# Performance work log

Hardware: AMD Instinct MI355X
Metric: run time of the kernel (lower is better)

Reference implementation:

```python
import jax, jax.numpy as jnp
import numpy as np

B = 8192
EMBED = 4  # self-attention embed dim


def setup_inputs() -> dict:
    key = jax.random.key(0)
    ks = jax.random.split(key, 20)
    f32 = jnp.float32
    return {
        "inputs": jax.random.normal(ks[0], (B, 8), dtype=f32),
        # MLP chain params (stored as [in, out]; y = x @ W + b)
        "W_fm": jax.random.normal(ks[1], (8, 16), dtype=f32) * 0.1,
        "b_fm": jnp.zeros((16,), dtype=f32),
        "W_c1": jax.random.normal(ks[2], (16, 16), dtype=f32) * 0.1,
        "b_c1": jnp.zeros((16,), dtype=f32),
        "W_p1": jax.random.normal(ks[3], (16, 12), dtype=f32) * 0.1,
        "b_p1": jnp.zeros((12,), dtype=f32),
        "W_c2": jax.random.normal(ks[4], (12, 8), dtype=f32) * 0.1,
        "b_c2": jnp.zeros((8,), dtype=f32),
        "W_p2": jax.random.normal(ks[5], (8, 4), dtype=f32) * 0.1,
        "b_p2": jnp.zeros((4,), dtype=f32),
        "W_c3": jax.random.normal(ks[6], (4, 4), dtype=f32) * 0.1,
        "b_c3": jnp.zeros((4,), dtype=f32),
        # self-attention params
        "rot": jax.random.normal(ks[7], (EMBED, EMBED), dtype=f32),
        "ent": jax.random.normal(ks[8], (EMBED, EMBED), dtype=f32),
        # ConvFilter: 2x2 conv kernel flattened (cross-correlation over 2x2 patch)
        "conv_w": jax.random.normal(ks[9], (4,), dtype=f32) * 0.5,
        "conv_b": jnp.zeros((1,), dtype=f32),
        # head: Linear(1,1)
        "head_w": jax.random.normal(ks[10], (1, 1), dtype=f32),
        "head_b": jnp.zeros((1,), dtype=f32),
    }


def reference(inputs, W_fm, b_fm, W_c1, b_c1, W_p1, b_p1, W_c2, b_c2,
              W_p2, b_p2, W_c3, b_c3, rot, ent, conv_w, conv_b,
              head_w, head_b):
    threshold = 0.0
    shift = 0.0
    # MLP chain: Linear + Tanh blocks
    x = jnp.tanh(inputs @ W_fm + b_fm)   # [B,16]
    x = jnp.tanh(x @ W_c1 + b_c1)        # [B,16]
    x = jnp.tanh(x @ W_p1 + b_p1)        # [B,12]
    x = jnp.tanh(x @ W_c2 + b_c2)        # [B,8]
    x = jnp.tanh(x @ W_p2 + b_p2)        # [B,4]
    x = jnp.tanh(x @ W_c3 + b_c3)        # [B,4]
    # self-attention over the batch axis (as in the original torch.mm)
    q = x @ rot                           # [B,4]
    k = x @ ent                           # [B,4]
    scores = jax.nn.softmax((q @ k.T) / jnp.sqrt(jnp.float32(EMBED)), axis=-1)  # [B,B]
    x = scores @ x                        # [B,4]
    # batched 2x2 conv filter: each sample's 4-vector reshaped to 2x2, one
    # valid conv output -> sum(w * patch) + b; mean of single elem is itself
    filtered = jax.nn.sigmoid(x @ conv_w + conv_b - threshold)[:, None]  # [B,1]
    logits = filtered @ head_w + head_b   # [B,1]
    return jax.nn.sigmoid(logits + shift)
```

## Files before the change

### kernel.cpp

```cpp
#include <hip/hip_runtime.h>
#include <math.h>

#define BATCH 8192
#define BLK 256
#define NSPLIT 32
#define CHUNK (BATCH / NSPLIT)


template <int IN, int OUT>
__device__ __forceinline__ void layer_tanh(const float* a, float* out,
                                           const float* __restrict__ W,
                                           const float* __restrict__ bias) {
  float acc[OUT];
#pragma unroll
  for (int o = 0; o < OUT; o++) acc[o] = bias[o];
#pragma unroll
  for (int i = 0; i < IN; i++) {
    float ai = a[i];
#pragma unroll
    for (int o = 0; o < OUT; o++) acc[o] = fmaf(ai, W[i * OUT + o], acc[o]);
  }
#pragma unroll
  for (int o = 0; o < OUT; o++) out[o] = tanhf(acc[o]);
}

__global__ __launch_bounds__(BLK) void mlp_kernel(
    const float* __restrict__ in,
    const float* __restrict__ W_fm, const float* __restrict__ b_fm,
    const float* __restrict__ W_c1, const float* __restrict__ b_c1,
    const float* __restrict__ W_p1, const float* __restrict__ b_p1,
    const float* __restrict__ W_c2, const float* __restrict__ b_c2,
    const float* __restrict__ W_p2, const float* __restrict__ b_p2,
    const float* __restrict__ W_c3, const float* __restrict__ b_c3,
    const float* __restrict__ rot, const float* __restrict__ ent,
    float4* __restrict__ qv, float4* __restrict__ kvx) {
  __shared__ float w[812];
  const int t = threadIdx.x;
  auto cp = [&](const float* src, int off, int n) {
    for (int i = t; i < n; i += BLK) w[off + i] = src[i];
  };
  cp(W_fm, 0, 128);  cp(b_fm, 128, 16);
  cp(W_c1, 144, 256); cp(b_c1, 400, 16);
  cp(W_p1, 416, 192); cp(b_p1, 608, 12);
  cp(W_c2, 620, 96);  cp(b_c2, 716, 8);
  cp(W_p2, 724, 32);  cp(b_p2, 756, 4);
  cp(W_c3, 760, 16);  cp(b_c3, 776, 4);
  cp(rot, 780, 16);   cp(ent, 796, 16);
  __syncthreads();

  const int r = blockIdx.x * BLK + t;
  const float4* in4 = (const float4*)in;
  float4 i0 = in4[r * 2 + 0];
  float4 i1 = in4[r * 2 + 1];
  float a[16], b[16];
  a[0] = i0.x; a[1] = i0.y; a[2] = i0.z; a[3] = i0.w;
  a[4] = i1.x; a[5] = i1.y; a[6] = i1.z; a[7] = i1.w;

  layer_tanh<8, 16>(a, b, w + 0, w + 128);
  layer_tanh<16, 16>(b, a, w + 144, w + 400);
  layer_tanh<16, 12>(a, b, w + 416, w + 608);
  layer_tanh<12, 8>(b, a, w + 620, w + 716);
  layer_tanh<8, 4>(a, b, w + 724, w + 756);
  layer_tanh<4, 4>(b, a, w + 760, w + 776);
  float q[4], k[4];
#pragma unroll
  for (int d = 0; d < 4; d++) {
    q[d] = a[0] * w[780 + 0 * 4 + d] + a[1] * w[780 + 1 * 4 + d] +
           a[2] * w[780 + 2 * 4 + d] + a[3] * w[780 + 3 * 4 + d];
    k[d] = a[0] * w[796 + 0 * 4 + d] + a[1] * w[796 + 1 * 4 + d] +
           a[2] * w[796 + 2 * 4 + d] + a[3] * w[796 + 3 * 4 + d];
  }
  qv[r] = make_float4(q[0] * 0.5f, q[1] * 0.5f, q[2] * 0.5f, q[3] * 0.5f);
  kvx[2 * r + 0] = make_float4(k[0], k[1], k[2], k[3]);
  kvx[2 * r + 1] = make_float4(a[0], a[1], a[2], a[3]);
}

__device__ __forceinline__ float dot4(float4 a, float4 b) {
  return fmaf(a.x, b.x, fmaf(a.y, b.y, fmaf(a.z, b.z, a.w * b.w)));
}

__global__ __launch_bounds__(BLK) void attn_partial(
    const float4* __restrict__ kvx, const float4* __restrict__ qv,
    float* __restrict__ l_arr, float4* __restrict__ o_arr) {
  const int t = threadIdx.x;
  const int qi = blockIdx.x * BLK + t;
  const int c0 = blockIdx.y * CHUNK;
  const float4 q = qv[qi];

  float l0 = 0.f, l1 = 0.f;
  float4 o0 = make_float4(0.f, 0.f, 0.f, 0.f);
  float4 o1 = make_float4(0.f, 0.f, 0.f, 0.f);
#pragma unroll 4
  for (int j = 0; j < CHUNK; j += 2) {
    const float4 ka = kvx[(c0 + j) * 2 + 0];
    const float4 va = kvx[(c0 + j) * 2 + 1];
    const float4 kb = kvx[(c0 + j) * 2 + 2];
    const float4 vb = kvx[(c0 + j) * 2 + 3];
    float s0 = dot4(q, ka);
    float s1 = dot4(q, kb);
    float p0 = __expf(s0);
    float p1 = __expf(s1);
    l0 += p0;
    l1 += p1;
    o0.x = fmaf(p0, va.x, o0.x); o0.y = fmaf(p0, va.y, o0.y);
    o0.z = fmaf(p0, va.z, o0.z); o0.w = fmaf(p0, va.w, o0.w);
    o1.x = fmaf(p1, vb.x, o1.x); o1.y = fmaf(p1, vb.y, o1.y);
    o1.z = fmaf(p1, vb.z, o1.z); o1.w = fmaf(p1, vb.w, o1.w);
  }
  const int idx = blockIdx.y * BATCH + qi;
  l_arr[idx] = l0 + l1;
  o_arr[idx] = make_float4(o0.x + o1.x, o0.y + o1.y, o0.z + o1.z, o0.w + o1.w);
}

__global__ __launch_bounds__(BLK) void combine_kernel(
    const float* __restrict__ l_arr, const float4* __restrict__ o_arr,
    const float* __restrict__ conv_w, const float* __restrict__ conv_b,
    const float* __restrict__ head_w, const float* __restrict__ head_b,
    float* __restrict__ out) {
  const int qi = blockIdx.x * BLK + threadIdx.x;
  float l = 0.f;
  float4 o = make_float4(0.f, 0.f, 0.f, 0.f);
#pragma unroll
  for (int s = 0; s < NSPLIT; s++) {
    l += l_arr[s * BATCH + qi];
    float4 os = o_arr[s * BATCH + qi];
    o.x += os.x; o.y += os.y; o.z += os.z; o.w += os.w;
  }
  const float inv = 1.0f / l;
  float z = o.x * inv * conv_w[0] + o.y * inv * conv_w[1] +
            o.z * inv * conv_w[2] + o.w * inv * conv_w[3] + conv_b[0];
  float filtered = 1.0f / (1.0f + __expf(-z));
  float logit = fmaf(filtered, head_w[0], head_b[0]);
  out[qi] = 1.0f / (1.0f + __expf(-logit));
}

extern "C" void kernel_launch(void* const* d_in, const int* in_sizes, int n_in,
                              void* d_out, int out_size, void* d_ws,
                              size_t ws_size, hipStream_t stream) {
  const float* in   = (const float*)d_in[0];
  const float* W_fm = (const float*)d_in[1];
  const float* b_fm = (const float*)d_in[2];
  const float* W_c1 = (const float*)d_in[3];
  const float* b_c1 = (const float*)d_in[4];
  const float* W_p1 = (const float*)d_in[5];
  const float* b_p1 = (const float*)d_in[6];
  const float* W_c2 = (const float*)d_in[7];
  const float* b_c2 = (const float*)d_in[8];
  const float* W_p2 = (const float*)d_in[9];
  const float* b_p2 = (const float*)d_in[10];
  const float* W_c3 = (const float*)d_in[11];
  const float* b_c3 = (const float*)d_in[12];
  const float* rot  = (const float*)d_in[13];
  const float* ent  = (const float*)d_in[14];
  const float* conv_w = (const float*)d_in[15];
  const float* conv_b = (const float*)d_in[16];
  const float* head_w = (const float*)d_in[17];
  const float* head_b = (const float*)d_in[18];
  float* out = (float*)d_out;

  char* ws = (char*)d_ws;
  float4* qv  = (float4*)(ws + 0);
  float4* kvx = (float4*)(ws + (128 << 10));
  float*  l_arr = (float*)(ws + (384 << 10));
  float4* o_arr = (float4*)(ws + (384 << 10) + NSPLIT * BATCH * 4);

  mlp_kernel<<<BATCH / BLK, BLK, 0, stream>>>(
      in, W_fm, b_fm, W_c1, b_c1, W_p1, b_p1, W_c2, b_c2, W_p2, b_p2, W_c3,
      b_c3, rot, ent, qv, kvx);

  dim3 grid(BATCH / BLK, NSPLIT);
  attn_partial<<<grid, BLK, 0, stream>>>(kvx, qv, l_arr, o_arr);

  combine_kernel<<<BATCH / BLK, BLK, 0, stream>>>(
      l_arr, o_arr, conv_w, conv_b, head_w, head_b, out);
}
```

Before: 128.3 us.

## Fuse MLP into attention kernel, recomputing query and key rows per block

Removes the separate MLP kernel. Each attention block now recomputes the MLP for its 256 query rows and its 256-key chunk, stages K/V in shared memory, and runs the partial softmax-weighted sum from LDS instead of global memory. tanhf is replaced by an exp/reciprocal approximation. Weights are read directly from global/scalar memory instead of shared memory, and launch bounds request 3 blocks per SM. The trade is redundant MLP compute (each row is recomputed 32 times as a query and 32 times as a key) in exchange for one fewer launch, no intermediate global traffic, and LDS-resident keys.

```diff
diff --git a/kernel.cpp b/kernel.cpp
--- a/kernel.cpp
+++ b/kernel.cpp
@@ -6,25 +6,44 @@
 #define NSPLIT 32
 #define CHUNK (BATCH / NSPLIT)
 
+__device__ __forceinline__ float tanh_fast(float x) {
+  float e = __expf(x + x);
+  return fmaf(-2.0f, __builtin_amdgcn_rcpf(e + 1.0f), 1.0f);
+}
 
 template <int IN, int OUT>
-__device__ __forceinline__ void layer_tanh(const float* a, float* out,
-                                           const float* __restrict__ W,
-                                           const float* __restrict__ bias) {
-  float acc[OUT];
+__device__ __forceinline__ void layer2_tanh(
+    const float* x0, const float* x1, float* y0, float* y1,
+    const float* __restrict__ W, const float* __restrict__ bias) {
+  float acc0[OUT], acc1[OUT];
 #pragma unroll
-  for (int o = 0; o < OUT; o++) acc[o] = bias[o];
+  for (int o = 0; o < OUT; o++) {
+    float b = bias[o];
+    acc0[o] = b;
+    acc1[o] = b;
+  }
 #pragma unroll
   for (int i = 0; i < IN; i++) {
-    float ai = a[i];
+    float a0 = x0[i], a1 = x1[i];
 #pragma unroll
-    for (int o = 0; o < OUT; o++) acc[o] = fmaf(ai, W[i * OUT + o], acc[o]);
+    for (int o = 0; o < OUT; o++) {
+      float w = W[i * OUT + o];
+      acc0[o] = fmaf(a0, w, acc0[o]);
+      acc1[o] = fmaf(a1, w, acc1[o]);
+    }
   }
 #pragma unroll
-  for (int o = 0; o < OUT; o++) out[o] = tanhf(acc[o]);
+  for (int o = 0; o < OUT; o++) {
+    y0[o] = tanh_fast(acc0[o]);
+    y1[o] = tanh_fast(acc1[o]);
+  }
 }
 
-__global__ __launch_bounds__(BLK) void mlp_kernel(
+__device__ __forceinline__ float dot4(float4 a, float4 b) {
+  return fmaf(a.x, b.x, fmaf(a.y, b.y, fmaf(a.z, b.z, a.w * b.w)));
+}
+
+__global__ __launch_bounds__(BLK, 3) void fused_attn(
     const float* __restrict__ in,
     const float* __restrict__ W_fm, const float* __restrict__ b_fm,
     const float* __restrict__ W_c1, const float* __restrict__ b_c1,
@@ -33,71 +52,57 @@
     const float* __restrict__ W_p2, const float* __restrict__ b_p2,
     const float* __restrict__ W_c3, const float* __restrict__ b_c3,
     const float* __restrict__ rot, const float* __restrict__ ent,
-    float4* __restrict__ qv, float4* __restrict__ kvx) {
-  __shared__ float w[812];
+    float* __restrict__ l_arr, float4* __restrict__ o_arr) {
+  __shared__ float4 kv[2 * CHUNK];
+
   const int t = threadIdx.x;
-  auto cp = [&](const float* src, int off, int n) {
-    for (int i = t; i < n; i += BLK) w[off + i] = src[i];
-  };
-  cp(W_fm, 0, 128);  cp(b_fm, 128, 16);
-  cp(W_c1, 144, 256); cp(b_c1, 400, 16);
-  cp(W_p1, 416, 192); cp(b_p1, 608, 12);
-  cp(W_c2, 620, 96);  cp(b_c2, 716, 8);
-  cp(W_p2, 724, 32);  cp(b_p2, 756, 4);
-  cp(W_c3, 760, 16);  cp(b_c3, 776, 4);
-  cp(rot, 780, 16);   cp(ent, 796, 16);
+  const int qi = blockIdx.x * BLK + t;
+  const int ki = blockIdx.y * CHUNK + t;
+
+  const float4* in4 = (const float4*)in;
+  float4 A0 = in4[2 * qi + 0], A1 = in4[2 * qi + 1];
+  float4 B0 = in4[2 * ki + 0], B1 = in4[2 * ki + 1];
+
+  float xq[16], tq[16], xk[16], tk[16];
+  xq[0] = A0.x; xq[1] = A0.y; xq[2] = A0.z; xq[3] = A0.w;
+  xq[4] = A1.x; xq[5] = A1.y; xq[6] = A1.z; xq[7] = A1.w;
+  xk[0] = B0.x; xk[1] = B0.y; xk[2] = B0.z; xk[3] = B0.w;
+  xk[4] = B1.x; xk[5] = B1.y; xk[6] = B1.z; xk[7] = B1.w;
+
+  layer2_tanh<8, 16>(xq, xk, tq, tk, W_fm, b_fm);
+  layer2_tanh<16, 16>(tq, tk, xq, xk, W_c1, b_c1);
+  layer2_tanh<16, 12>(xq, xk, tq, tk, W_p1, b_p1);
+  layer2_tanh<12, 8>(tq, tk, xq, xk, W_c2, b_c2);
+  layer2_tanh<8, 4>(xq, xk, tq, tk, W_p2, b_p2);
+  layer2_tanh<4, 4>(tq, tk, xq, xk, W_c3, b_c3);
+
+  float qd[4], kd[4];
+#pragma unroll
+  for (int d = 0; d < 4; d++) {
+    qd[d] = xq[0] * rot[0 * 4 + d] + xq[1] * rot[1 * 4 + d] +
+            xq[2] * rot[2 * 4 + d] + xq[3] * rot[3 * 4 + d];
+    kd[d] = xk[0] * ent[0 * 4 + d] + xk[1] * ent[1 * 4 + d] +
+            xk[2] * ent[2 * 4 + d] + xk[3] * ent[3 * 4 + d];
+  }
+
+  kv[2 * t + 0] = make_float4(kd[0], kd[1], kd[2], kd[3]);
+  kv[2 * t + 1] = make_float4(xk[0], xk[1], xk[2], xk[3]);
   __syncthreads();
 
-  const int r = blockIdx.x * BLK + t;
-  const float4* in4 = (const float4*)in;
-  float4 i0 = in4[r * 2 + 0];
-  float4 i1 = in4[r * 2 + 1];
-  float a[16], b[16];
-  a[0] = i0.x; a[1] = i0.y; a[2] = i0.z; a[3] = i0.w;
-  a[4] = i1.x; a[5] = i1.y; a[6] = i1.z; a[7] = i1.w;
-
-  layer_tanh<8, 16>(a, b, w + 0, w + 128);
-  layer_tanh<16, 16>(b, a, w + 144, w + 400);
-  layer_tanh<16, 12>(a, b, w + 416, w + 608);
-  layer_tanh<12, 8>(b, a, w + 620, w + 716);
-  layer_tanh<8, 4>(a, b, w + 724, w + 756);
-  layer_tanh<4, 4>(b, a, w + 760, w + 776);
-  float q[4], k[4];
-#pragma unroll
-  for (int d = 0; d < 4; d++) {
-    q[d] = a[0] * w[780 + 0 * 4 + d] + a[1] * w[780 + 1 * 4 + d] +
-           a[2] * w[780 + 2 * 4 + d] + a[3] * w[780 + 3 * 4 + d];
-    k[d] = a[0] * w[796 + 0 * 4 + d] + a[1] * w[796 + 1 * 4 + d] +
-           a[2] * w[796 + 2 * 4 + d] + a[3] * w[796 + 3 * 4 + d];
-  }
-  qv[r] = make_float4(q[0] * 0.5f, q[1] * 0.5f, q[2] * 0.5f, q[3] * 0.5f);
-  kvx[2 * r + 0] = make_float4(k[0], k[1], k[2], k[3]);
-  kvx[2 * r + 1] = make_float4(a[0], a[1], a[2], a[3]);
-}
-
-__device__ __forceinline__ float dot4(float4 a, float4 b) {
-  return fmaf(a.x, b.x, fmaf(a.y, b.y, fmaf(a.z, b.z, a.w * b.w)));
-}
-
-__global__ __launch_bounds__(BLK) void attn_partial(
-    const float4* __restrict__ kvx, const float4* __restrict__ qv,
-    float* __restrict__ l_arr, float4* __restrict__ o_arr) {
-  const int t = threadIdx.x;
-  const int qi = blockIdx.x * BLK + t;
-  const int c0 = blockIdx.y * CHUNK;
-  const float4 q = qv[qi];
+  const float4 Q =
+      make_float4(qd[0] * 0.5f, qd[1] * 0.5f, qd[2] * 0.5f, qd[3] * 0.5f);
 
   float l0 = 0.f, l1 = 0.f;
   float4 o0 = make_float4(0.f, 0.f, 0.f, 0.f);
   float4 o1 = make_float4(0.f, 0.f, 0.f, 0.f);
 #pragma unroll 4
   for (int j = 0; j < CHUNK; j += 2) {
-    const float4 ka = kvx[(c0 + j) * 2 + 0];
-    const float4 va = kvx[(c0 + j) * 2 + 1];
-    const float4 kb = kvx[(c0 + j) * 2 + 2];
-    const float4 vb = kvx[(c0 + j) * 2 + 3];
-    float s0 = dot4(q, ka);
-    float s1 = dot4(q, kb);
+    const float4 ka = kv[2 * j + 0];
+    const float4 va = kv[2 * j + 1];
+    const float4 kb = kv[2 * j + 2];
+    const float4 vb = kv[2 * j + 3];
+    float s0 = dot4(Q, ka);
+    float s1 = dot4(Q, kb);
     float p0 = __expf(s0);
     float p1 = __expf(s1);
     l0 += p0;
@@ -159,17 +164,13 @@
   float* out = (float*)d_out;
 
   char* ws = (char*)d_ws;
-  float4* qv  = (float4*)(ws + 0);
-  float4* kvx = (float4*)(ws + (128 << 10));
-  float*  l_arr = (float*)(ws + (384 << 10));
-  float4* o_arr = (float4*)(ws + (384 << 10) + NSPLIT * BATCH * 4);
-
-  mlp_kernel<<<BATCH / BLK, BLK, 0, stream>>>(
-      in, W_fm, b_fm, W_c1, b_c1, W_p1, b_p1, W_c2, b_c2, W_p2, b_p2, W_c3,
-      b_c3, rot, ent, qv, kvx);
+  float*  l_arr = (float*)ws;
+  float4* o_arr = (float4*)(ws + (size_t)NSPLIT * BATCH * 4);
 
   dim3 grid(BATCH / BLK, NSPLIT);
-  attn_partial<<<grid, BLK, 0, stream>>>(kvx, qv, l_arr, o_arr);
+  fused_attn<<<grid, BLK, 0, stream>>>(
+      in, W_fm, b_fm, W_c1, b_c1, W_p1, b_p1, W_c2, b_c2, W_p2, b_p2, W_c3,
+      b_c3, rot, ent, l_arr, o_arr);
 
   combine_kernel<<<BATCH / BLK, BLK, 0, stream>>>(
       l_arr, o_arr, conv_w, conv_b, head_w, head_b, out);
```

New measurement: 130.0 us. About the same (+1.3%).
